# Optimization experiments

Hardware: AMD Instinct MI355X
Metric: run time of the kernel (lower is better)

The kernel has to match this reference:

```python
import jax, jax.numpy as jnp
import numpy as np

N, E, G = 20000, 320000, 256      # nodes, edges, graphs per batch
IN, D, P = 128, 256, 16           # input_dim, out_dim, n_prot
EPS, R, TEMP = 1e-7, 0.5, 0.2


def setup_inputs() -> dict:
    key = jax.random.key(0)
    ks = jax.random.split(key, 9)
    x = jax.random.normal(ks[0], (N, IN), jnp.float32)
    edge_index = jax.random.randint(ks[1], (2, E), 0, N)
    batch = jnp.sort(jax.random.randint(ks[2], (N,), 0, G))
    def w(k, sh):
        fan_in = sh[0]
        return jax.random.normal(k, sh, jnp.float32) * (1.0 / fan_in) ** 0.5
    return {
        "x": x, "edge_index": edge_index, "batch": batch,
        "W1": w(ks[3], (IN, D)), "b1": jnp.zeros((D,), jnp.float32),
        "W2": w(ks[4], (D, D)), "b2": jnp.zeros((D,), jnp.float32),
        "Wm1": w(ks[5], (2 * D, D)), "bm1": jnp.zeros((D,), jnp.float32),
        "Wm2": w(ks[6], (D, 1)), "bm2": jnp.zeros((1,), jnp.float32),
        "prototypes": jax.random.normal(ks[7], (P, D), jnp.float32),
    }


def _cosine(a, b):
    # prototype_distances: cosine similarity with zero-norm -> eps fixup (eval path, no softmax)
    na = jnp.linalg.norm(a, axis=1)
    na = jnp.where(na == 0, na + EPS, na)
    nb = jnp.linalg.norm(b, axis=1)
    nb = jnp.where(nb == 0, nb + EPS, nb)
    return jnp.einsum('ik,jk->ij', a, b) / (na[:, None] * nb[None, :])


def _encoder(x, src, dst, batch, W1, b1, W2, b2, atten=None):
    # 2-layer GIN: h' = relu((h + sum_{j->i} atten_ji * h_j) W + b); graph emb = sum pool
    def conv(h, W, b):
        msg = h[src]                                   # [E, d]
        if atten is not None:
            msg = msg * atten                          # [E, 1] broadcast
        agg = h + jax.ops.segment_sum(msg, dst, num_segments=N)
        return jax.nn.relu(agg @ W + b)
    h = conv(x, W1, b1)
    h = conv(h, W2, b2)
    g = jax.ops.segment_sum(h, batch, num_segments=G)  # [G, D]
    return g, h


def reference(x, edge_index, batch, W1, b1, W2, b2, Wm1, bm1, Wm2, bm2, prototypes):
    src, dst = edge_index[0], edge_index[1]
    graph_embs, node_embs = _encoder(x, src, dst, batch, W1, b1, W2, b2)

    # eval path: assign each graph to nearest prototype by cosine similarity
    sim0 = _cosine(graph_embs, prototypes)             # [G, P]
    assign_prot = jnp.argmax(sim0, axis=1)             # [G]

    # sample_subgraph (eval: plain sigmoid, no gumbel noise)
    node_proto = prototypes[assign_prot[batch]]        # [N, D]
    h = jnp.concatenate([node_embs, node_proto], axis=-1)
    node_prob = jax.nn.relu(h @ Wm1 + bm1) @ Wm2 + bm2  # [N, 1]
    node_bern = jax.nn.sigmoid(node_prob)              # [N, 1]
    edge_bern = node_bern[src] * node_bern[dst]        # [E, 1]

    x2 = x * node_bern
    subgraph_embs, _ = _encoder(x2, src, dst, batch, W1, b1, W2, b2, atten=edge_bern)

    similarity = _cosine(subgraph_embs, prototypes)    # [G, P]

    # NCE loss
    a2 = jnp.argmax(similarity, axis=1)
    onehot = jax.nn.one_hot(a2, P, dtype=similarity.dtype)
    se = jnp.exp(similarity / TEMP)
    pos = (se * onehot).sum(axis=1)
    neg = (se * (1.0 - onehot)).sum(axis=1)
    NCE_loss = -jnp.log(pos / neg).mean()

    # KL regularizers
    nb = node_bern
    KL_node = (nb * jnp.log(nb / R + EPS)
               + (1 - nb) * jnp.log((1 - nb) / (1 - R + EPS) + EPS)).mean()
    eb = edge_bern
    KL_edge = (eb * jnp.log(eb / (R * R) + EPS)
               + (1 - eb) * jnp.log((1 - eb) / (1 - R * R + EPS) + EPS)).mean()
    KL_loss = KL_node + KL_edge

    data_sim = _cosine(subgraph_embs, subgraph_embs)   # [G, G]
    return (KL_loss, NCE_loss, similarity, node_bern, edge_bern,
            data_sim, subgraph_embs, node_embs)
```

## Files before the change

### kernel.cpp

```cpp
#include <hip/hip_runtime.h>
#include <cmath>
#include <cstdint>

#define DINL __device__ __forceinline__

namespace {

constexpr int Nn = 20000, Ee = 320000, Gg = 256, Dd = 256, Pp = 16;
constexpr int Npad = 20096;
constexpr float EPSf = 1e-7f, Rf = 0.5f, TEMPf = 0.2f;

typedef unsigned short u16;
typedef __attribute__((ext_vector_type(8))) short short8;
typedef __attribute__((ext_vector_type(4))) float floatx4;
typedef __attribute__((ext_vector_type(2))) unsigned int u2v;
typedef __attribute__((ext_vector_type(4))) unsigned int u4v;

DINL float waveSum(float x) {
#pragma unroll
  for (int off = 32; off > 0; off >>= 1) x += __shfl_xor(x, off, 64);
  return x;
}

DINL u16 f2bf(float f) {
  unsigned u = __float_as_uint(f);
  unsigned r = u + 0x7fffu + ((u >> 16) & 1u);
  return (u16)(r >> 16);
}
DINL float bf2f(u16 h) { return __uint_as_float(((unsigned)h) << 16); }

__global__ void k_deg(const int* __restrict__ dst, int* __restrict__ deg) {
  int e = blockIdx.x * 256 + threadIdx.x;
  if (e < Ee) atomicAdd(&deg[dst[e]], 1);
}

__global__ __launch_bounds__(1024) void k_pre(const int* __restrict__ deg,
                                              int* __restrict__ offs,
                                              const int* __restrict__ batch,
                                              int* __restrict__ goff) {
  int tid = threadIdx.x;
  if (blockIdx.x == 0) {
    __shared__ int part[1024];
    const int chunk = (Nn + 1023) >> 10;
    int start = tid * chunk;
    int s = 0;
    for (int k = 0; k < chunk; k++) { int i = start + k; if (i < Nn) s += deg[i]; }
    part[tid] = s;
    __syncthreads();
    for (int off = 1; off < 1024; off <<= 1) {
      int v = (tid >= off) ? part[tid - off] : 0;
      __syncthreads();
      part[tid] += v;
      __syncthreads();
    }
    int run = (tid == 0) ? 0 : part[tid - 1];
    for (int k = 0; k < chunk; k++) {
      int i = start + k;
      if (i < Nn) { offs[i] = run; run += deg[i]; }
    }
    if (start < Nn && start + chunk >= Nn) offs[Nn] = run;
  } else {
    for (int i = tid; i < Nn; i += 1024) {
      int bi = batch[i];
      int bp = (i == 0) ? -1 : batch[i - 1];
      for (int g = bp + 1; g <= bi; ++g) goff[g] = i;
      if (i == Nn - 1)
        for (int g = bi + 1; g <= Gg; ++g) goff[g] = Nn;
    }
  }
}

__global__ void k_fill(const int* __restrict__ src, const int* __restrict__ dst,
                       const int* __restrict__ offs, int* __restrict__ cursor,
                       int* __restrict__ csr) {
  int e = blockIdx.x * 256 + threadIdx.x;
  if (e < Ee) {
    int d = dst[e];
    int pos = atomicAdd(&cursor[d], 1);
    csr[offs[d] + pos] = src[e];
  }
}

template <int DIM, int EPL, bool INBF>
DINL void slice(float r[EPL], const void* __restrict__ hv, int row, int ce) {
  if constexpr (INBF) {
    const u16* p = (const u16*)hv + (size_t)row * DIM + ce;
    ushort4 u = *(const ushort4*)p;
    r[0] = bf2f(u.x); r[1] = bf2f(u.y); r[2] = bf2f(u.z); r[3] = bf2f(u.w);
  } else {
    const float* p = (const float*)hv + (size_t)row * DIM + ce;
    float2 u = *(const float2*)p;
    r[0] = u.x; r[1] = u.y;
  }
}

template <int DIM, int MODE, bool INBF, bool OSPL>
__global__ __launch_bounds__(256) void k_aggc(
    const void* __restrict__ hv, const float* __restrict__ nb,
    const int* __restrict__ offs, const int* __restrict__ csr,
    u16* __restrict__ oh, u16* __restrict__ ol) {
  constexpr int EPL = INBF ? 4 : 2;
  constexpr int COLS = EPL * 16;
  constexpr int CHUNKS = DIM / COLS;
  int c = (int)(blockIdx.x % CHUNKS);
  int grp = (int)(blockIdx.x / CHUNKS);
  int wv = threadIdx.x >> 6, lane = threadIdx.x & 63;
  int sub = lane >> 4, l = lane & 15;
  int node = grp * 16 + wv * 4 + sub;
  if (node >= Nn) return;
  int ce = c * COLS + l * EPL;
  float self[EPL], ts[EPL];
  slice<DIM, EPL, INBF>(self, hv, node, ce);
#pragma unroll
  for (int j = 0; j < EPL; j++) ts[j] = 0.f;
  int beg = offs[node], end = offs[node + 1];
  int k = beg;
  for (; k + 4 <= end; k += 4) {
    int s0 = csr[k], s1 = csr[k + 1], s2 = csr[k + 2], s3 = csr[k + 3];
    float r0[EPL], r1[EPL], r2[EPL], r3[EPL];
    slice<DIM, EPL, INBF>(r0, hv, s0, ce);
    slice<DIM, EPL, INBF>(r1, hv, s1, ce);
    slice<DIM, EPL, INBF>(r2, hv, s2, ce);
    slice<DIM, EPL, INBF>(r3, hv, s3, ce);
    if (MODE == 0) {
#pragma unroll
      for (int j = 0; j < EPL; j++) ts[j] += (r0[j] + r1[j]) + (r2[j] + r3[j]);
    } else {
      float w0 = nb[s0], w1 = nb[s1], w2 = nb[s2], w3 = nb[s3];
      if (MODE == 1) { w0 *= w0; w1 *= w1; w2 *= w2; w3 *= w3; }
#pragma unroll
      for (int j = 0; j < EPL; j++)
        ts[j] += (w0 * r0[j] + w1 * r1[j]) + (w2 * r2[j] + w3 * r3[j]);
    }
  }
  for (; k < end; k++) {
    int s = csr[k];
    float r[EPL];
    slice<DIM, EPL, INBF>(r, hv, s, ce);
    if (MODE == 0) {
#pragma unroll
      for (int j = 0; j < EPL; j++) ts[j] += r[j];
    } else {
      float wq = nb[s];
      if (MODE == 1) wq *= wq;
#pragma unroll
      for (int j = 0; j < EPL; j++) ts[j] += wq * r[j];
    }
  }
  float val[EPL];
  if (MODE == 0) {
#pragma unroll
    for (int j = 0; j < EPL; j++) val[j] = self[j] + ts[j];
  } else if (MODE == 1) {
    float wi = nb[node];
#pragma unroll
    for (int j = 0; j < EPL; j++) val[j] = wi * (self[j] + ts[j]);
  } else {
    float wi = nb[node];
#pragma unroll
    for (int j = 0; j < EPL; j++) val[j] = self[j] + wi * ts[j];
  }
  u16 hs[EPL], ls[EPL];
#pragma unroll
  for (int j = 0; j < EPL; j++) {
    hs[j] = f2bf(val[j]);
    if (OSPL) ls[j] = f2bf(val[j] - bf2f(hs[j]));
  }
  u16* po = oh + (size_t)node * DIM + ce;
  if constexpr (EPL == 2) {
    unsigned v = (unsigned)hs[0] | ((unsigned)hs[1] << 16);
    __builtin_nontemporal_store(v, (unsigned*)po);
  } else {
    u2v v;
    v.x = (unsigned)hs[0] | ((unsigned)hs[1] << 16);
    v.y = (unsigned)hs[2] | ((unsigned)hs[3] << 16);
    __builtin_nontemporal_store(v, (u2v*)po);
  }
  if constexpr (OSPL) {
    u16* pl = ol + (size_t)node * DIM + ce;
    if constexpr (EPL == 2) {
      unsigned v = (unsigned)ls[0] | ((unsigned)ls[1] << 16);
      __builtin_nontemporal_store(v, (unsigned*)pl);
    } else {
      u2v v;
      v.x = (unsigned)ls[0] | ((unsigned)ls[1] << 16);
      v.y = (unsigned)ls[2] | ((unsigned)ls[3] << 16);
      __builtin_nontemporal_store(v, (u2v*)pl);
    }
  }
}

template <int K, bool SPLIT, int MODE>
__global__ __launch_bounds__(256) void k_mm(
    const u16* __restrict__ Ah, const u16* __restrict__ Al,
    const u16* __restrict__ Bh, const u16* __restrict__ Bl,
    const float* __restrict__ bias,
    float* __restrict__ outF, u16* __restrict__ outH, u16* __restrict__ outL,
    const float* __restrict__ pc, const int* __restrict__ batch,
    const int* __restrict__ assign, const float* __restrict__ Wm2,
    float* __restrict__ prob) {
  constexpr int SK = 40;
  __shared__ u16 AsH[64 * SK];
  __shared__ u16 AsL[SPLIT ? 64 * SK : 16];
  __shared__ u16 BsH[64 * SK];
  __shared__ u16 BsL[SPLIT ? 64 * SK : 16];
  __shared__ int ap_s[64];
  int t = threadIdx.x;
  int rowBase = blockIdx.y * 64, colBase = blockIdx.x * 64;
  if (MODE == 1 && t < 64) {
    int r = rowBase + t;
    ap_s[t] = (r < Nn) ? assign[batch[r]] : 0;
  }
  int lane = t & 63, wv = t >> 6;
  int quad = lane >> 4, l16 = lane & 15;
  int wm = wv * 16;
  floatx4 acc[4];
#pragma unroll
  for (int nt = 0; nt < 4; nt++) acc[nt] = (floatx4){0.f, 0.f, 0.f, 0.f};

  int ar = t >> 2;
  int ak = (t & 3) * 8;
  const u16* agH = Ah + (size_t)(rowBase + ar) * K + ak;
  const u16* agL = Al + (size_t)(rowBase + ar) * K + ak;
  const u16* bgH = Bh + (size_t)(colBase + ar) * K + ak;
  const u16* bgL = Bl + (size_t)(colBase + ar) * K + ak;

  u4v cAH = *(const u4v*)(agH);
  u4v cBH = *(const u4v*)(bgH);
  u4v cAL, cBL;
  if constexpr (SPLIT) {
    cAL = *(const u4v*)(agL);
    cBL = *(const u4v*)(bgL);
  }

  for (int k0 = 0; k0 < K; k0 += 32) {
    __syncthreads();
    *(u4v*)&AsH[ar * SK + ak] = cAH;
    *(u4v*)&BsH[ar * SK + ak] = cBH;
    if constexpr (SPLIT) {
      *(u4v*)&AsL[ar * SK + ak] = cAL;
      *(u4v*)&BsL[ar * SK + ak] = cBL;
    }
    __syncthreads();
    if (k0 + 32 < K) {
      cAH = *(const u4v*)(agH + k0 + 32);
      cBH = *(const u4v*)(bgH + k0 + 32);
      if constexpr (SPLIT) {
        cAL = *(const u4v*)(agL + k0 + 32);
        cBL = *(const u4v*)(bgL + k0 + 32);
      }
    }
    int aoff = (wm + l16) * SK + quad * 8;
    short8 aH = *(const short8*)&AsH[aoff];
    short8 aL;
    if constexpr (SPLIT) aL = *(const short8*)&AsL[aoff];
#pragma unroll
    for (int nt = 0; nt < 4; nt++) {
      int boff = (nt * 16 + l16) * SK + quad * 8;
      short8 bH = *(const short8*)&BsH[boff];
      acc[nt] = __builtin_amdgcn_mfma_f32_16x16x32_bf16(aH, bH, acc[nt], 0, 0, 0);
      if constexpr (SPLIT) {
        short8 bL = *(const short8*)&BsL[boff];
        acc[nt] = __builtin_amdgcn_mfma_f32_16x16x32_bf16(aH, bL, acc[nt], 0, 0, 0);
        acc[nt] = __builtin_amdgcn_mfma_f32_16x16x32_bf16(aL, bH, acc[nt], 0, 0, 0);
      }
    }
  }

  if constexpr (MODE == 0) {
#pragma unroll
    for (int nt = 0; nt < 4; nt++) {
      int col = colBase + nt * 16 + l16;
      float bv = bias[col];
#pragma unroll
      for (int r = 0; r < 4; r++) {
        int row = rowBase + wm + quad * 4 + r;
        if (row < Nn) {
          float v = fmaxf(acc[nt][r] + bv, 0.f);
          size_t o = (size_t)row * 256 + col;
          if (outF) outF[o] = v;
          if (outH) {
            u16 hh = f2bf(v);
            outH[o] = hh;
            if (outL) outL[o] = f2bf(v - bf2f(hh));
          }
        }
      }
    }
  } else {
    float part[4] = {0.f, 0.f, 0.f, 0.f};
#pragma unroll
    for (int nt = 0; nt < 4; nt++) {
      int col = colBase + nt * 16 + l16;
      float wmv = Wm2[col];
#pragma unroll
      for (int r = 0; r < 4; r++) {
        int ap = ap_s[wm + quad * 4 + r];
        float tv = fmaxf(acc[nt][r] + pc[ap * 256 + col], 0.f);
        part[r] += tv * wmv;
      }
    }
#pragma unroll
    for (int r = 0; r < 4; r++) {
#pragma unroll
      for (int off = 1; off < 16; off <<= 1) part[r] += __shfl_xor(part[r], off, 64);
      if (l16 == 0) {
        int row = rowBase + wm + quad * 4 + r;
        if (row < Nn) atomicAdd(&prob[row], part[r]);
      }
    }
  }
}

__global__ __launch_bounds__(256) void k_poolassign(
    const float* __restrict__ h, const int* __restrict__ goff,
    const float* __restrict__ proto, const float* __restrict__ pnorm,
    int* __restrict__ assign) {
  __shared__ float row[Dd];
  int g = blockIdx.x, c = threadIdx.x;
  int beg = goff[g], end = goff[g + 1];
  float s = 0.f;
  for (int n = beg; n < end; ++n)
    s += __builtin_nontemporal_load(&h[(size_t)n * Dd + c]);
  row[c] = s;
  __syncthreads();
  if (c < 64) {
    float4 v = ((const float4*)row)[c];
    float na = sqrtf(waveSum(v.x * v.x + v.y * v.y + v.z * v.z + v.w * v.w));
    if (na == 0.f) na = EPSf;
    float best = -1e30f;
    int bi = 0;
#pragma unroll
    for (int p = 0; p < Pp; p++) {
      float4 w = *(const float4*)(proto + (size_t)p * Dd + c * 4);
      float d = waveSum(v.x * w.x + v.y * w.y + v.z * w.z + v.w * w.w);
      float sim = d / (na * pnorm[p]);
      if (sim > best) { best = sim; bi = p; }
    }
    if (c == 0) assign[g] = bi;
  }
}

__global__ __launch_bounds__(256) void k_poolsim(
    const float* __restrict__ h, const int* __restrict__ goff,
    const float* __restrict__ proto, const float* __restrict__ pnorm,
    float* __restrict__ o_sg, float* __restrict__ sgemb,
    float* __restrict__ osim, float* __restrict__ snorm,
    float* __restrict__ nceAcc) {
  __shared__ float row[Dd];
  int g = blockIdx.x, c = threadIdx.x;
  int beg = goff[g], end = goff[g + 1];
  float s = 0.f;
  for (int n = beg; n < end; ++n)
    s += __builtin_nontemporal_load(&h[(size_t)n * Dd + c]);
  row[c] = s;
  o_sg[(size_t)g * Dd + c] = s;
  sgemb[(size_t)g * Dd + c] = s;
  __syncthreads();
  if (c < 64) {
    float4 v = ((const float4*)row)[c];
    float na = sqrtf(waveSum(v.x * v.x + v.y * v.y + v.z * v.z + v.w * v.w));
    if (na == 0.f) na = EPSf;
    float sims[Pp];
#pragma unroll
    for (int p = 0; p < Pp; p++) {
      float4 w = *(const float4*)(proto + (size_t)p * Dd + c * 4);
      float d = waveSum(v.x * w.x + v.y * w.y + v.z * w.z + v.w * w.w);
      float sim = d / (na * pnorm[p]);
      sims[p] = sim;
      if (c == p) osim[g * Pp + p] = sim;
    }
    float best = sims[0];
    int bi = 0;
#pragma unroll
    for (int p = 1; p < Pp; p++) {
      if (sims[p] > best) { best = sims[p]; bi = p; }
    }
    float pos = 0.f, neg = 0.f;
#pragma unroll
    for (int p = 0; p < Pp; p++) {
      float e = expf(sims[p] / TEMPf);
      if (p == bi) pos = e; else neg += e;
    }
    if (c == 0) {
      atomicAdd(nceAcc, -logf(pos / neg));
      snorm[g] = na;
    }
  }
}

__global__ __launch_bounds__(64) void k_pc(const float* __restrict__ proto,
                                           const float* __restrict__ Wm1,
                                           const float* __restrict__ bm1,
                                           float* __restrict__ pc,
                                           float* __restrict__ pnorm) {
  int p = blockIdx.x, q = blockIdx.y, t = threadIdx.x;
  int cc = q * 64 + t;
  float s = bm1[cc];
  for (int k = 0; k < Dd; k++) s += proto[p * Dd + k] * Wm1[(size_t)(Dd + k) * Dd + cc];
  pc[p * Dd + cc] = s;
  if (q == 0) {
    float4 v = ((const float4*)(proto + (size_t)p * Dd))[t];
    float nsq = waveSum(v.x * v.x + v.y * v.y + v.z * v.z + v.w * v.w);
    if (t == 0) {
      float n = sqrtf(nsq);
      pnorm[p] = (n == 0.f) ? EPSf : n;
    }
  }
}

__global__ void k_berneb(const float* __restrict__ prob, const float* __restrict__ bm2,
                         const int* __restrict__ src, const int* __restrict__ dst,
                         const float* __restrict__ x, u16* __restrict__ xbf,
                         float* __restrict__ ob, float* __restrict__ oe,
                         float* __restrict__ accs) {
  const int nB = (Nn + 255) / 256, eB = (Ee + 255) / 256;
  int b = blockIdx.x;
  if (b < nB) {
    int i = b * 256 + threadIdx.x;
    float val = 0.f;
    if (i < Nn) {
      float z = prob[i] + bm2[0];
      float p = 1.f / (1.f + expf(-z));
      ob[i] = p;
      const float invA = 1.f / Rf, invB = 1.f / (1.f - Rf + EPSf);
      val = p * logf(p * invA + EPSf) + (1.f - p) * logf((1.f - p) * invB + EPSf);
    }
    val = waveSum(val);
    __shared__ float wsum[4];
    int lane = threadIdx.x & 63, wvv = threadIdx.x >> 6;
    if (lane == 0) wsum[wvv] = val;
    __syncthreads();
    if (threadIdx.x == 0) atomicAdd(accs, wsum[0] + wsum[1] + wsum[2] + wsum[3]);
  } else if (b < nB + eB) {
    int e = (b - nB) * 256 + threadIdx.x;
    float val = 0.f;
    if (e < Ee) {
      float zs = prob[src[e]] + bm2[0];
      float zd = prob[dst[e]] + bm2[0];
      float ps = 1.f / (1.f + expf(-zs));
      float pd = 1.f / (1.f + expf(-zd));
      float v = ps * pd;
      __builtin_nontemporal_store(v, &oe[e]);
      const float invA = 1.f / (Rf * Rf), invB = 1.f / (1.f - Rf * Rf + EPSf);
      val = v * logf(v * invA + EPSf) + (1.f - v) * logf((1.f - v) * invB + EPSf);
    }
    val = waveSum(val);
    __shared__ float wsum2[4];
    int lane = threadIdx.x & 63, wvv = threadIdx.x >> 6;
    if (lane == 0) wsum2[wvv] = val;
    __syncthreads();
    if (threadIdx.x == 0) atomicAdd(accs + 1, wsum2[0] + wsum2[1] + wsum2[2] + wsum2[3]);
  } else {
    int i = (b - nB - eB) * 256 + threadIdx.x;
    if (i < Nn * 128 / 4) {
      float4 v = ((const float4*)x)[i];
      u2v o;
      o.x = (unsigned)f2bf(v.x) | ((unsigned)f2bf(v.y) << 16);
      o.y = (unsigned)f2bf(v.z) | ((unsigned)f2bf(v.w) << 16);
      __builtin_nontemporal_store(o, (u2v*)&xbf[(size_t)i * 4]);
    }
  }
}

__global__ void k_fin(const float* __restrict__ accs, float* __restrict__ o_kl,
                      float* __restrict__ o_nce) {
  o_kl[0] = accs[0] / (float)Nn + accs[1] / (float)Ee;
  o_nce[0] = accs[2] / (float)Gg;
}

__global__ void k_datasim(const float* __restrict__ S, const float* __restrict__ snorm,
                          float* __restrict__ out) {
  __shared__ float si[Dd];
  int i = blockIdx.x, j = threadIdx.x;
  si[j] = S[(size_t)i * Dd + j];
  __syncthreads();
  const float4* rj = (const float4*)(S + (size_t)j * Dd);
  const float4* sif = (const float4*)si;
  float d = 0.f;
#pragma unroll 4
  for (int k = 0; k < Dd / 4; k++) {
    float4 a = sif[k];
    float4 b = rj[k];
    d += a.x * b.x + a.y * b.y + a.z * b.z + a.w * b.w;
  }
  out[(size_t)i * Gg + j] = d / (snorm[i] * snorm[j]);
}

__global__ void k_prep(const float* __restrict__ W1, const float* __restrict__ W2,
                       const float* __restrict__ Wm1, u16* __restrict__ W1th,
                       u16* __restrict__ W1tl, u16* __restrict__ W2th,
                       u16* __restrict__ W2tl, u16* __restrict__ Wm1th,
                       u16* __restrict__ Wm1tl) {
  int idx = blockIdx.x * 256 + threadIdx.x;
  const float* W;
  u16 *th, *tl;
  int K;
  if (idx < 128 * 256) {
    W = W1; th = W1th; tl = W1tl; K = 128;
  } else if (idx < 128 * 256 + 256 * 256) {
    idx -= 128 * 256;
    W = W2; th = W2th; tl = W2tl; K = 256;
  } else {
    idx -= 128 * 256 + 256 * 256;
    if (idx >= 256 * 256) return;
    W = Wm1; th = Wm1th; tl = Wm1tl; K = 256;
  }
  int k = idx >> 8, n = idx & 255;
  float v = W[idx];
  u16 h = f2bf(v);
  th[(size_t)n * K + k] = h;
  tl[(size_t)n * K + k] = f2bf(v - bf2f(h));
}

}

extern "C" void kernel_launch(void* const* d_in, const int* in_sizes, int n_in,
                              void* d_out, int out_size, void* d_ws, size_t ws_size,
                              hipStream_t stream) {
  const float* x = (const float*)d_in[0];
  const int* ei = (const int*)d_in[1];
  const int* batch = (const int*)d_in[2];
  const float* W1 = (const float*)d_in[3];
  const float* b1 = (const float*)d_in[4];
  const float* W2 = (const float*)d_in[5];
  const float* b2 = (const float*)d_in[6];
  const float* Wm1 = (const float*)d_in[7];
  const float* bm1 = (const float*)d_in[8];
  const float* Wm2 = (const float*)d_in[9];
  const float* bm2 = (const float*)d_in[10];
  const float* proto = (const float*)d_in[11];
  const int* src = ei;
  const int* dst = ei + Ee;

  float* out = (float*)d_out;
  float* o_kl = out;
  float* o_nce = out + 1;
  float* o_sim = out + 2;
  float* o_nb = o_sim + Gg * Pp;
  float* o_eb = o_nb + Nn;
  float* o_ds = o_eb + Ee;
  float* o_sg = o_ds + Gg * Gg;
  float* o_ne = o_sg + Gg * Dd;

  char* w = (char*)d_ws;
  auto take = [&](size_t bytes) -> char* {
    char* p = w;
    w += (bytes + 255) & ~(size_t)255;
    return p;
  };
  const size_t halfR = (size_t)Npad * 256 * 2;
  float* bufB = (float*)take((size_t)Npad * 256 * 4);
  char* R2 = take(2 * halfR);
  u16* A1h = (u16*)R2;
  u16* A1l = (u16*)(R2 + (size_t)Npad * 128 * 2);
  u16* A2h = (u16*)R2;
  u16* A2l = (u16*)(R2 + halfR);
  u16* h1b = (u16*)R2;
  u16* a2bh = (u16*)(R2 + halfR);
  char* R3 = take(2 * halfR);
  u16* neh = (u16*)R3;
  u16* nel = (u16*)(R3 + halfR);
  u16* a1bh = (u16*)R3;
  u16* xbf = (u16*)(R3 + halfR);

  int* csr = (int*)take((size_t)Ee * 4);
  int* deg = (int*)take((size_t)Nn * 4);
  int* cursor = (int*)take((size_t)Nn * 4);
  int* offs = (int*)take((size_t)(Nn + 1) * 4);
  int* goff = (int*)take((size_t)(Gg + 1) * 4);
  float* sgemb = (float*)take((size_t)Gg * Dd * 4);
  float* pcb = (float*)take((size_t)Pp * Dd * 4);
  float* pnorm = (float*)take(Pp * 4);
  int* assign = (int*)take(Gg * 4);
  float* snorm = (float*)take(Gg * 4);
  float* prob = (float*)take(Nn * 4);
  float* accs = (float*)take(16);
  u16* W1th = (u16*)take((size_t)256 * 128 * 2);
  u16* W1tl = (u16*)take((size_t)256 * 128 * 2);
  u16* W2th = (u16*)take((size_t)256 * 256 * 2);
  u16* W2tl = (u16*)take((size_t)256 * 256 * 2);
  u16* Wm1th = (u16*)take((size_t)256 * 256 * 2);
  u16* Wm1tl = (u16*)take((size_t)256 * 256 * 2);

  hipMemsetAsync(deg, 0, 2 * 80128, stream);
  hipMemsetAsync(prob, 0, 80128 + 16, stream);

  const int eB = (Ee + 255) / 256;
  const int nB = (Nn + 255) / 256;
  dim3 gmm(4, 314);

  k_deg<<<eB, 256, 0, stream>>>(dst, deg);
  k_pre<<<2, 1024, 0, stream>>>(deg, offs, batch, goff);
  k_fill<<<eB, 256, 0, stream>>>(src, dst, offs, cursor, csr);
  k_pc<<<dim3(Pp, 4), 64, 0, stream>>>(proto, Wm1, bm1, pcb, pnorm);
  k_prep<<<640, 256, 0, stream>>>(W1, W2, Wm1, W1th, W1tl, W2th, W2tl, Wm1th, Wm1tl);

  k_aggc<128, 0, false, true><<<1250 * 4, 256, 0, stream>>>(x, nullptr, offs, csr, A1h, A1l);
  k_mm<128, true, 0><<<gmm, 256, 0, stream>>>(A1h, A1l, W1th, W1tl, b1, bufB, nullptr,
                                              nullptr, nullptr, nullptr, nullptr,
                                              nullptr, nullptr);
  k_aggc<256, 0, false, true><<<1250 * 8, 256, 0, stream>>>(bufB, nullptr, offs, csr, A2h, A2l);
  k_mm<256, true, 0><<<gmm, 256, 0, stream>>>(A2h, A2l, W2th, W2tl, b2, o_ne, neh, nel,
                                              nullptr, nullptr, nullptr, nullptr,
                                              nullptr);
  k_poolassign<<<Gg, 256, 0, stream>>>(o_ne, goff, proto, pnorm, assign);
  k_mm<256, true, 1><<<gmm, 256, 0, stream>>>(neh, nel, Wm1th, Wm1tl, nullptr, nullptr,
                                              nullptr, nullptr, pcb, batch, assign,
                                              Wm2, prob);
  k_berneb<<<nB + eB + (Nn * 128 / 4 + 255) / 256, 256, 0, stream>>>(
      prob, bm2, src, dst, x, xbf, o_nb, o_eb, accs);

  k_aggc<128, 1, true, false><<<1250 * 2, 256, 0, stream>>>(xbf, o_nb, offs, csr, a1bh, nullptr);
  k_mm<128, false, 0><<<gmm, 256, 0, stream>>>(a1bh, nullptr, W1th, nullptr, b1, nullptr,
                                               h1b, nullptr, nullptr, nullptr, nullptr,
                                               nullptr, nullptr);
  k_aggc<256, 2, true, false><<<1250 * 4, 256, 0, stream>>>(h1b, o_nb, offs, csr, a2bh, nullptr);
  k_mm<256, false, 0><<<gmm, 256, 0, stream>>>(a2bh, nullptr, W2th, nullptr, b2, bufB,
                                               nullptr, nullptr, nullptr, nullptr,
                                               nullptr, nullptr, nullptr);
  k_poolsim<<<Gg, 256, 0, stream>>>(bufB, goff, proto, pnorm, o_sg, sgemb, o_sim, snorm,
                                    accs + 2);
  k_fin<<<1, 1, 0, stream>>>(accs, o_kl, o_nce);
  k_datasim<<<Gg, 256, 0, stream>>>(sgemb, snorm, o_ds);
}
```

Measured before the change: 447.0 us.

## Use persistent XCC-restricted work-stealing aggregation blocks and fold final scalar kernel

Measured after the change: 679.9 us. +52.1%, slower.

```diff
diff --git a/kernel.cpp b/kernel.cpp
--- a/kernel.cpp
+++ b/kernel.cpp
@@ -98,94 +98,109 @@
 __global__ __launch_bounds__(256) void k_aggc(
     const void* __restrict__ hv, const float* __restrict__ nb,
     const int* __restrict__ offs, const int* __restrict__ csr,
-    u16* __restrict__ oh, u16* __restrict__ ol) {
+    u16* __restrict__ oh, u16* __restrict__ ol, int* __restrict__ ctr) {
   constexpr int EPL = INBF ? 4 : 2;
   constexpr int COLS = EPL * 16;
   constexpr int CHUNKS = DIM / COLS;
-  int c = (int)(blockIdx.x % CHUNKS);
-  int grp = (int)(blockIdx.x / CHUNKS);
+  constexpr int NGRP = 157;
+  constexpr int TOTAL = CHUNKS * NGRP;
+  int xcc;
+  asm volatile("s_getreg_b32 %0, hwreg(HW_REG_XCC_ID)" : "=s"(xcc));
+  if (!((blockIdx.x < 32) || ((xcc & 7) < 4))) return;
+  __shared__ int s_item;
   int wv = threadIdx.x >> 6, lane = threadIdx.x & 63;
   int sub = lane >> 4, l = lane & 15;
-  int node = grp * 16 + wv * 4 + sub;
-  if (node >= Nn) return;
-  int ce = c * COLS + l * EPL;
-  float self[EPL], ts[EPL];
-  slice<DIM, EPL, INBF>(self, hv, node, ce);
-#pragma unroll
-  for (int j = 0; j < EPL; j++) ts[j] = 0.f;
-  int beg = offs[node], end = offs[node + 1];
-  int k = beg;
-  for (; k + 4 <= end; k += 4) {
-    int s0 = csr[k], s1 = csr[k + 1], s2 = csr[k + 2], s3 = csr[k + 3];
-    float r0[EPL], r1[EPL], r2[EPL], r3[EPL];
-    slice<DIM, EPL, INBF>(r0, hv, s0, ce);
-    slice<DIM, EPL, INBF>(r1, hv, s1, ce);
-    slice<DIM, EPL, INBF>(r2, hv, s2, ce);
-    slice<DIM, EPL, INBF>(r3, hv, s3, ce);
-    if (MODE == 0) {
-#pragma unroll
-      for (int j = 0; j < EPL; j++) ts[j] += (r0[j] + r1[j]) + (r2[j] + r3[j]);
-    } else {
-      float w0 = nb[s0], w1 = nb[s1], w2 = nb[s2], w3 = nb[s3];
-      if (MODE == 1) { w0 *= w0; w1 *= w1; w2 *= w2; w3 *= w3; }
-#pragma unroll
-      for (int j = 0; j < EPL; j++)
-        ts[j] += (w0 * r0[j] + w1 * r1[j]) + (w2 * r2[j] + w3 * r3[j]);
-    }
-  }
-  for (; k < end; k++) {
-    int s = csr[k];
-    float r[EPL];
-    slice<DIM, EPL, INBF>(r, hv, s, ce);
-    if (MODE == 0) {
-#pragma unroll
-      for (int j = 0; j < EPL; j++) ts[j] += r[j];
-    } else {
-      float wq = nb[s];
-      if (MODE == 1) wq *= wq;
-#pragma unroll
-      for (int j = 0; j < EPL; j++) ts[j] += wq * r[j];
-    }
-  }
-  float val[EPL];
-  if (MODE == 0) {
-#pragma unroll
-    for (int j = 0; j < EPL; j++) val[j] = self[j] + ts[j];
-  } else if (MODE == 1) {
-    float wi = nb[node];
-#pragma unroll
-    for (int j = 0; j < EPL; j++) val[j] = wi * (self[j] + ts[j]);
-  } else {
-    float wi = nb[node];
-#pragma unroll
-    for (int j = 0; j < EPL; j++) val[j] = self[j] + wi * ts[j];
-  }
-  u16 hs[EPL], ls[EPL];
-#pragma unroll
-  for (int j = 0; j < EPL; j++) {
-    hs[j] = f2bf(val[j]);
-    if (OSPL) ls[j] = f2bf(val[j] - bf2f(hs[j]));
-  }
-  u16* po = oh + (size_t)node * DIM + ce;
-  if constexpr (EPL == 2) {
-    unsigned v = (unsigned)hs[0] | ((unsigned)hs[1] << 16);
-    __builtin_nontemporal_store(v, (unsigned*)po);
-  } else {
-    u2v v;
-    v.x = (unsigned)hs[0] | ((unsigned)hs[1] << 16);
-    v.y = (unsigned)hs[2] | ((unsigned)hs[3] << 16);
-    __builtin_nontemporal_store(v, (u2v*)po);
-  }
-  if constexpr (OSPL) {
-    u16* pl = ol + (size_t)node * DIM + ce;
-    if constexpr (EPL == 2) {
-      unsigned v = (unsigned)ls[0] | ((unsigned)ls[1] << 16);
-      __builtin_nontemporal_store(v, (unsigned*)pl);
-    } else {
-      u2v v;
-      v.x = (unsigned)ls[0] | ((unsigned)ls[1] << 16);
-      v.y = (unsigned)ls[2] | ((unsigned)ls[3] << 16);
-      __builtin_nontemporal_store(v, (u2v*)pl);
+  for (;;) {
+    __syncthreads();
+    if (threadIdx.x == 0) s_item = atomicAdd(ctr, 1);
+    __syncthreads();
+    int item = s_item;
+    if (item >= TOTAL) return;
+    int c = item / NGRP;
+    int g0 = (item % NGRP) * 128;
+    int ce = c * COLS + l * EPL;
+    for (int nn = 0; nn < 8; nn++) {
+      int node = g0 + nn * 16 + wv * 4 + sub;
+      if (node >= Nn) continue;
+      float self[EPL], ts[EPL];
+      slice<DIM, EPL, INBF>(self, hv, node, ce);
+#pragma unroll
+      for (int j = 0; j < EPL; j++) ts[j] = 0.f;
+      int beg = offs[node], end = offs[node + 1];
+      int k = beg;
+      for (; k + 4 <= end; k += 4) {
+        int s0 = csr[k], s1 = csr[k + 1], s2 = csr[k + 2], s3 = csr[k + 3];
+        float r0[EPL], r1[EPL], r2[EPL], r3[EPL];
+        slice<DIM, EPL, INBF>(r0, hv, s0, ce);
+        slice<DIM, EPL, INBF>(r1, hv, s1, ce);
+        slice<DIM, EPL, INBF>(r2, hv, s2, ce);
+        slice<DIM, EPL, INBF>(r3, hv, s3, ce);
+        if (MODE == 0) {
+#pragma unroll
+          for (int j = 0; j < EPL; j++) ts[j] += (r0[j] + r1[j]) + (r2[j] + r3[j]);
+        } else {
+          float w0 = nb[s0], w1 = nb[s1], w2 = nb[s2], w3 = nb[s3];
+          if (MODE == 1) { w0 *= w0; w1 *= w1; w2 *= w2; w3 *= w3; }
+#pragma unroll
+          for (int j = 0; j < EPL; j++)
+            ts[j] += (w0 * r0[j] + w1 * r1[j]) + (w2 * r2[j] + w3 * r3[j]);
+        }
+      }
+      for (; k < end; k++) {
+        int s = csr[k];
+        float r[EPL];
+        slice<DIM, EPL, INBF>(r, hv, s, ce);
+        if (MODE == 0) {
+#pragma unroll
+          for (int j = 0; j < EPL; j++) ts[j] += r[j];
+        } else {
+          float wq = nb[s];
+          if (MODE == 1) wq *= wq;
+#pragma unroll
+          for (int j = 0; j < EPL; j++) ts[j] += wq * r[j];
+        }
+      }
+      float val[EPL];
+      if (MODE == 0) {
+#pragma unroll
+        for (int j = 0; j < EPL; j++) val[j] = self[j] + ts[j];
+      } else if (MODE == 1) {
+        float wi = nb[node];
+#pragma unroll
+        for (int j = 0; j < EPL; j++) val[j] = wi * (self[j] + ts[j]);
+      } else {
+        float wi = nb[node];
+#pragma unroll
+        for (int j = 0; j < EPL; j++) val[j] = self[j] + wi * ts[j];
+      }
+      u16 hs[EPL], ls[EPL];
+#pragma unroll
+      for (int j = 0; j < EPL; j++) {
+        hs[j] = f2bf(val[j]);
+        if (OSPL) ls[j] = f2bf(val[j] - bf2f(hs[j]));
+      }
+      u16* po = oh + (size_t)node * DIM + ce;
+      if constexpr (EPL == 2) {
+        unsigned v = (unsigned)hs[0] | ((unsigned)hs[1] << 16);
+        __builtin_nontemporal_store(v, (unsigned*)po);
+      } else {
+        u2v v;
+        v.x = (unsigned)hs[0] | ((unsigned)hs[1] << 16);
+        v.y = (unsigned)hs[2] | ((unsigned)hs[3] << 16);
+        __builtin_nontemporal_store(v, (u2v*)po);
+      }
+      if constexpr (OSPL) {
+        u16* pl = ol + (size_t)node * DIM + ce;
+        if constexpr (EPL == 2) {
+          unsigned v = (unsigned)ls[0] | ((unsigned)ls[1] << 16);
+          __builtin_nontemporal_store(v, (unsigned*)pl);
+        } else {
+          u2v v;
+          v.x = (unsigned)ls[0] | ((unsigned)ls[1] << 16);
+          v.y = (unsigned)ls[2] | ((unsigned)ls[3] << 16);
+          __builtin_nontemporal_store(v, (u2v*)pl);
+        }
+      }
     }
   }
 }
@@ -463,16 +478,15 @@
   }
 }
 
-__global__ void k_fin(const float* __restrict__ accs, float* __restrict__ o_kl,
-                      float* __restrict__ o_nce) {
-  o_kl[0] = accs[0] / (float)Nn + accs[1] / (float)Ee;
-  o_nce[0] = accs[2] / (float)Gg;
-}
-
 __global__ void k_datasim(const float* __restrict__ S, const float* __restrict__ snorm,
-                          float* __restrict__ out) {
+                          float* __restrict__ out, const float* __restrict__ accs,
+                          float* __restrict__ o_kl, float* __restrict__ o_nce) {
+  int i = blockIdx.x, j = threadIdx.x;
+  if (i == 0 && j == 0) {
+    o_kl[0] = accs[0] / (float)Nn + accs[1] / (float)Ee;
+    o_nce[0] = accs[2] / (float)Gg;
+  }
   __shared__ float si[Dd];
-  int i = blockIdx.x, j = threadIdx.x;
   si[j] = S[(size_t)i * Dd + j];
   __syncthreads();
   const float4* rj = (const float4*)(S + (size_t)j * Dd);
@@ -576,6 +590,7 @@
   float* snorm = (float*)take(Gg * 4);
   float* prob = (float*)take(Nn * 4);
   float* accs = (float*)take(16);
+  int* ctrs = (int*)take(16);
   u16* W1th = (u16*)take((size_t)256 * 128 * 2);
   u16* W1tl = (u16*)take((size_t)256 * 128 * 2);
   u16* W2th = (u16*)take((size_t)256 * 256 * 2);
@@ -584,11 +599,12 @@
   u16* Wm1tl = (u16*)take((size_t)256 * 256 * 2);
 
   hipMemsetAsync(deg, 0, 2 * 80128, stream);
-  hipMemsetAsync(prob, 0, 80128 + 16, stream);
+  hipMemsetAsync(prob, 0, 80128 + 512, stream);
 
   const int eB = (Ee + 255) / 256;
   const int nB = (Nn + 255) / 256;
   dim3 gmm(4, 314);
+  const int aggB = 2048;
 
   k_deg<<<eB, 256, 0, stream>>>(dst, deg);
   k_pre<<<2, 1024, 0, stream>>>(deg, offs, batch, goff);
@@ -596,11 +612,13 @@
   k_pc<<<dim3(Pp, 4), 64, 0, stream>>>(proto, Wm1, bm1, pcb, pnorm);
   k_prep<<<640, 256, 0, stream>>>(W1, W2, Wm1, W1th, W1tl, W2th, W2tl, Wm1th, Wm1tl);
 
-  k_aggc<128, 0, false, true><<<1250 * 4, 256, 0, stream>>>(x, nullptr, offs, csr, A1h, A1l);
+  k_aggc<128, 0, false, true><<<aggB, 256, 0, stream>>>(x, nullptr, offs, csr, A1h, A1l,
+                                                        ctrs + 0);
   k_mm<128, true, 0><<<gmm, 256, 0, stream>>>(A1h, A1l, W1th, W1tl, b1, bufB, nullptr,
                                               nullptr, nullptr, nullptr, nullptr,
                                               nullptr, nullptr);
-  k_aggc<256, 0, false, true><<<1250 * 8, 256, 0, stream>>>(bufB, nullptr, offs, csr, A2h, A2l);
+  k_aggc<256, 0, false, true><<<aggB, 256, 0, stream>>>(bufB, nullptr, offs, csr, A2h,
+                                                        A2l, ctrs + 1);
   k_mm<256, true, 0><<<gmm, 256, 0, stream>>>(A2h, A2l, W2th, W2tl, b2, o_ne, neh, nel,
                                               nullptr, nullptr, nullptr, nullptr,
                                               nullptr);
@@ -611,16 +629,17 @@
   k_berneb<<<nB + eB + (Nn * 128 / 4 + 255) / 256, 256, 0, stream>>>(
       prob, bm2, src, dst, x, xbf, o_nb, o_eb, accs);
 
-  k_aggc<128, 1, true, false><<<1250 * 2, 256, 0, stream>>>(xbf, o_nb, offs, csr, a1bh, nullptr);
+  k_aggc<128, 1, true, false><<<aggB, 256, 0, stream>>>(xbf, o_nb, offs, csr, a1bh,
+                                                        nullptr, ctrs + 2);
   k_mm<128, false, 0><<<gmm, 256, 0, stream>>>(a1bh, nullptr, W1th, nullptr, b1, nullptr,
                                                h1b, nullptr, nullptr, nullptr, nullptr,
                                                nullptr, nullptr);
-  k_aggc<256, 2, true, false><<<1250 * 4, 256, 0, stream>>>(h1b, o_nb, offs, csr, a2bh, nullptr);
+  k_aggc<256, 2, true, false><<<aggB, 256, 0, stream>>>(h1b, o_nb, offs, csr, a2bh,
+                                                        nullptr, ctrs + 3);
   k_mm<256, false, 0><<<gmm, 256, 0, stream>>>(a2bh, nullptr, W2th, nullptr, b2, bufB,
                                                nullptr, nullptr, nullptr, nullptr,
                                                nullptr, nullptr, nullptr);
   k_poolsim<<<Gg, 256, 0, stream>>>(bufB, goff, proto, pnorm, o_sg, sgemb, o_sim, snorm,
                                     accs + 2);
-  k_fin<<<1, 1, 0, stream>>>(accs, o_kl, o_nce);
-  k_datasim<<<Gg, 256, 0, stream>>>(sgemb, snorm, o_ds);
-}
+  k_datasim<<<Gg, 256, 0, stream>>>(sgemb, snorm, o_ds, accs, o_kl, o_nce);
+}
```
